# Kernel tuning notes

Measured on AMD Instinct MI355X. Metric: run time of the kernel, lower is better.

The kernel has to match this reference:

```python
import jax, jax.numpy as jnp
import numpy as np

INPUT_DIM = 1024
NUM_HEADS = 16


def setup_inputs() -> dict:
    key = jax.random.key(0)
    k1, k2, k3, k4, k5, k6, k7, k8 = jax.random.split(key, 8)
    bs, seq, dm = 2, 2048, INPUT_DIM
    scale = 1.0 / np.sqrt(dm)
    return {
        "input": jax.random.normal(k1, (bs, seq, dm), dtype=jnp.float32),
        "mask": jax.random.randint(k2, (bs, seq), 0, 2, dtype=jnp.int32),
        "Wq": jax.random.normal(k3, (dm, dm), dtype=jnp.float32) * scale,
        "bq": jax.random.normal(k4, (dm,), dtype=jnp.float32) * 0.01,
        "Wk": jax.random.normal(k5, (dm, dm), dtype=jnp.float32) * scale,
        "bk": jax.random.normal(k6, (dm,), dtype=jnp.float32) * 0.01,
        "Wv": jax.random.normal(k7, (dm, dm), dtype=jnp.float32) * scale,
        "bv": jax.random.normal(k8, (dm,), dtype=jnp.float32) * 0.01,
    }


def reference(input, mask, Wq, bq, Wk, bk, Wv, bv):
    bs, seq, dm = input.shape
    h = NUM_HEADS
    d = dm // h
    # projections: x @ W^T + b (torch Linear convention)
    Q = (input @ Wq.T + bq).reshape(bs, seq, h, d).transpose(0, 2, 1, 3)
    K = (input @ Wk.T + bk).reshape(bs, seq, h, d).transpose(0, 2, 1, 3)
    V = (input @ Wv.T + bv).reshape(bs, seq, h, d).transpose(0, 2, 1, 3)
    # raw scores [bs, h, seq, seq]
    scores = jnp.einsum("bhqd,bhkd->bhqk", Q, K)
    m = mask.astype(jnp.float32).reshape(bs, 1, 1, seq)
    # mask_logits is applied BEFORE the 1/sqrt(d) scaling, as in source
    scores = scores * m + (1.0 - m) * (-1e30)
    scores = scores * (1.0 / np.sqrt(d))
    attn = jax.nn.softmax(scores, axis=-1)  # dropout = identity at eval
    out = jnp.einsum("bhqk,bhkd->bhqd", attn, V)
    return out.transpose(0, 2, 1, 3).reshape(bs, seq, dm)
```

## Files before the change

kernel.cpp:

```cpp
#include <hip/hip_runtime.h>
#include <stdint.h>
#include <stddef.h>

#define SEQ 2048
#define DM  1024
#define NH  16
#define BS  2
#define PPAD 72

typedef __attribute__((ext_vector_type(8)))  __bf16 bf16x8;
typedef __attribute__((ext_vector_type(4)))  __bf16 bf16x4;
typedef __attribute__((ext_vector_type(4)))  float  floatx4;
typedef __attribute__((ext_vector_type(16))) float  floatx16;
typedef __attribute__((ext_vector_type(4)))  unsigned int uintx4;
typedef __attribute__((ext_vector_type(4)))  unsigned short ushortx4;

#if __has_builtin(__builtin_amdgcn_exp2f)
#define EXP2(x) __builtin_amdgcn_exp2f(x)
#else
#define EXP2(x) __expf((x) * 0.6931471805599453f)
#endif

#define QSCALE 0.18033688011112042f
#define MBIAS_OK (-11.541560327111707f)

#define GLDS(g, s) __builtin_amdgcn_global_load_lds( \
    (const __attribute__((address_space(1))) void*)(g), \
    (__attribute__((address_space(3))) void*)(s), 16, 0, 0)

__device__ inline unsigned short f2bf(float f) {
  union { float f; unsigned int u; } a; a.f = f;
  unsigned int u = a.u;
  return (unsigned short)((u + 0x7fffu + ((u >> 16) & 1u)) >> 16);
}

__device__ inline bf16x8 ldb8(const unsigned short* p) { return *(const bf16x8*)p; }

__global__ __launch_bounds__(256) void prep(
    const float* __restrict__ x, const float* __restrict__ wq,
    const float* __restrict__ wk, const float* __restrict__ wv,
    const int* __restrict__ mask,
    unsigned short* __restrict__ Xb, unsigned short* __restrict__ Wb,
    float* __restrict__ mbias) {
  const int bid = blockIdx.x, t = threadIdx.x;
  if (bid < 7168) {
    const float* src; unsigned short* dst; int base;
    if (bid < 4096)      { src = x;  dst = Xb;            base = bid; }
    else if (bid < 5120) { src = wq; dst = Wb;            base = bid - 4096; }
    else if (bid < 6144) { src = wk; dst = Wb + 1048576;  base = bid - 5120; }
    else                 { src = wv; dst = Wb + 2097152;  base = bid - 6144; }
    const int i = base * 256 + t;
    floatx4 v = ((const floatx4*)src)[i];
    ushortx4 o;
    o.x = f2bf(v.x); o.y = f2bf(v.y); o.z = f2bf(v.z); o.w = f2bf(v.w);
    ((ushortx4*)dst)[i] = o;
  } else {
    const int i = (bid - 7168) * 256 + t;
    mbias[i] = mask[i] ? MBIAS_OK : -1.0e30f;
  }
}

__global__ __launch_bounds__(256, 3) void gemm_qkv(
    const unsigned short* __restrict__ Xb, const unsigned short* __restrict__ Wb,
    const float* __restrict__ bq, const float* __restrict__ bk, const float* __restrict__ bv,
    unsigned short* __restrict__ Qb, unsigned short* __restrict__ Kb,
    unsigned short* __restrict__ Vt)
{
  __shared__ alignas(16) unsigned short LB[16384];
  const int t = threadIdx.x;
  const int w = t >> 6, l = t & 63;
  const int lm = l & 15, lq = l >> 4;
  const int z = blockIdx.z;
  const size_t m0 = (size_t)blockIdx.y * 128;
  const size_t n0 = (size_t)blockIdx.x * 128;
  const unsigned short* W = Wb + (size_t)z * (1024 * 1024);
  const float* bias = (z == 0) ? bq : ((z == 1) ? bk : bv);
  const float sc = (z == 0) ? QSCALE : 1.0f;

  const int c0 = t, c1 = 256 + t;
  const int row0 = c0 >> 2, row1 = c1 >> 2;
  const int kq0 = (c0 & 3) ^ ((row0 >> 1) & 3);
  const int kq1 = (c1 & 3) ^ ((row1 >> 1) & 3);
  const unsigned short* gA0 = Xb + (m0 + row0) * 1024 + kq0 * 8;
  const unsigned short* gA1 = Xb + (m0 + row1) * 1024 + kq1 * 8;
  const unsigned short* gB0 = W + (n0 + row0) * 1024 + kq0 * 8;
  const unsigned short* gB1 = W + (n0 + row1) * 1024 + kq1 * 8;
  const int la0 = (0 * 256 + w * 64) * 8;
  const int la1 = (1 * 256 + w * 64) * 8;

  const int wr = (w >> 1) * 64, wc = (w & 1) * 64;
  const int sw = (lq ^ ((lm >> 1) & 3)) * 8;
  floatx4 acc[4][4] = {};

  GLDS(gA0, LB + la0);
  GLDS(gA1, LB + la1);
  GLDS(gB0, LB + 8192 + la0);
  GLDS(gB1, LB + 8192 + la1);
  __syncthreads();

  for (int it = 0; it < 32; ++it) {
    const int cur = it & 1;
    if (it < 31) {
      const int kn = (it + 1) * 32;
      const int nb = (cur ^ 1) * 4096;
      GLDS(gA0 + kn, LB + nb + la0);
      GLDS(gA1 + kn, LB + nb + la1);
      GLDS(gB0 + kn, LB + 8192 + nb + la0);
      GLDS(gB1 + kn, LB + 8192 + nb + la1);
    }
    const unsigned short* Ab = LB + cur * 4096;
    const unsigned short* Bb = LB + 8192 + cur * 4096;
    bf16x8 af[4], bfr[4];
#pragma unroll
    for (int i = 0; i < 4; i++) af[i] = ldb8(Ab + (wr + i * 16 + lm) * 32 + sw);
#pragma unroll
    for (int j = 0; j < 4; j++) bfr[j] = ldb8(Bb + (wc + j * 16 + lm) * 32 + sw);
#pragma unroll
    for (int i = 0; i < 4; i++)
#pragma unroll
      for (int j = 0; j < 4; j++)
        acc[i][j] = __builtin_amdgcn_mfma_f32_16x16x32_bf16(af[i], bfr[j], acc[i][j], 0, 0, 0);
    __syncthreads();
  }

  if (z < 2) {
    unsigned short* dst = (z == 0) ? Qb : Kb;
#pragma unroll
    for (int j = 0; j < 4; j++) {
      const int ncol = (int)n0 + wc + j * 16 + lm;
      const float bval = bias[ncol];
#pragma unroll
      for (int i = 0; i < 4; i++)
#pragma unroll
        for (int r = 0; r < 4; r++) {
          const int mrow = (int)m0 + wr + i * 16 + lq * 4 + r;
          dst[(size_t)mrow * 1024 + ncol] = f2bf((acc[i][j][r] + bval) * sc);
        }
    }
  } else {
#pragma unroll
    for (int j = 0; j < 4; j++) {
      const int nl = wc + j * 16 + lm;
      const float bval = bias[(int)n0 + nl];
#pragma unroll
      for (int i = 0; i < 4; i++)
#pragma unroll
        for (int r = 0; r < 4; r++) {
          const int ml = wr + i * 16 + lq * 4 + r;
          LB[nl * 128 + ((((ml >> 3) ^ (nl & 15)) * 8) | (ml & 7))] = f2bf(acc[i][j][r] + bval);
        }
    }
    __syncthreads();
    const int nl = t >> 1, hf = t & 1;
    const int ncol = (int)n0 + nl;
    const int hh = ncol >> 6, dc = ncol & 63;
    const int bb = (int)(m0 >> 11);
    const int s0c = ((int)m0 & 2047) + hf * 64;
    unsigned short* dstp = Vt + (size_t)((bb * 16 + hh) * 64 + dc) * SEQ + s0c;
#pragma unroll
    for (int u = 0; u < 8; ++u) {
      const int phys = (hf * 8 + u) ^ (nl & 15);
      *(uintx4*)(dstp + u * 8) = *(const uintx4*)(LB + nl * 128 + phys * 8);
    }
  }
}

__global__ __launch_bounds__(256, 2) void attn(
    const unsigned short* __restrict__ Qb, const unsigned short* __restrict__ Kb,
    const unsigned short* __restrict__ Vt, const float* __restrict__ mbias,
    float* __restrict__ out)
{
  __shared__ alignas(16) unsigned short Klds[2][4096];
  __shared__ alignas(16) unsigned short Vlds[2][4096];
  __shared__ alignas(16) unsigned short Plds[4][32 * PPAD];
  __shared__ alignas(16) float Mlds[SEQ];

  const int t = threadIdx.x, w = t >> 6, l = t & 63;
  const int ln = l & 31, h = l >> 5;
  const int bid = blockIdx.x;
  const int pp = bid & 31;
  const int b = pp >> 4, head = pp & 15;
  const int q0w = (bid >> 5) * 128 + w * 32;
  const int hoff = head * 64;

  const int sr = l >> 3;
  const int gc = (l & 7) ^ sr;
  const unsigned short* gK[2]; const unsigned short* gV[2];
#pragma unroll
  for (int s2 = 0; s2 < 2; ++s2) {
    const int row = w * 16 + s2 * 8 + sr;
    gK[s2] = Kb + (size_t)(b * SEQ + row) * DM + hoff + gc * 8;
    gV[s2] = Vt + (size_t)((b * NH + head) * 64 + row) * SEQ + gc * 8;
  }

#pragma unroll
  for (int s2 = 0; s2 < 2; ++s2) {
    GLDS(gK[s2], &Klds[0][(w * 128 + s2 * 64) * 8]);
    GLDS(gV[s2], &Vlds[0][(w * 128 + s2 * 64) * 8]);
  }

  {
    const floatx4* mb4 = (const floatx4*)(mbias + b * SEQ);
    ((floatx4*)Mlds)[t] = mb4[t];
    ((floatx4*)Mlds)[256 + t] = mb4[256 + t];
  }

  const unsigned short* Qbase = Qb + (size_t)(b * SEQ + q0w + ln) * DM + hoff + h * 8;
  bf16x8 qf[4];
#pragma unroll
  for (int c = 0; c < 4; ++c) qf[c] = ldb8(Qbase + c * 16);

  const int cc = (ln >> 1) & 3, hb = h ^ (ln & 1);
  int xoff[4];
#pragma unroll
  for (int c = 0; c < 4; ++c) xoff[c] = (c ^ cc) * 16 + hb * 8;

  unsigned short* P = &Plds[w][ln * PPAD];
  floatx16 oacc[2] = {};
  float tsum = 0.0f;

  __syncthreads();

  for (int kt = 0; kt < 32; ++kt) {
    const int cur = kt & 1;
    if (kt < 31) {
      const int k0n = (kt + 1) * 64;
#pragma unroll
      for (int s2 = 0; s2 < 2; ++s2) {
        GLDS(gK[s2] + (size_t)k0n * DM, &Klds[cur ^ 1][(w * 128 + s2 * 64) * 8]);
        GLDS(gV[s2] + k0n,              &Vlds[cur ^ 1][(w * 128 + s2 * 64) * 8]);
      }
    }
    const unsigned short* Kc = &Klds[cur][ln * 64];
    const unsigned short* Vc = &Vlds[cur][ln * 64];

    bf16x8 kfr[8], vfr[8];
#pragma unroll
    for (int i = 0; i < 8; ++i) {
      kfr[i] = ldb8(Kc + (i >> 2) * 2048 + xoff[i & 3]);
      vfr[i] = ldb8(Vc + (i >> 2) * 2048 + xoff[i & 3]);
    }

    floatx16 s[2] = {};
#pragma unroll
    for (int c = 0; c < 4; ++c) {
      s[0] = __builtin_amdgcn_mfma_f32_32x32x16_bf16(kfr[c],     qf[c], s[0], 0, 0, 0);
      s[1] = __builtin_amdgcn_mfma_f32_32x32x16_bf16(kfr[4 + c], qf[c], s[1], 0, 0, 0);
    }

    const int k0 = kt * 64;
#pragma unroll
    for (int kb = 0; kb < 2; ++kb)
#pragma unroll
      for (int g = 0; g < 4; ++g) {
        const floatx4 mbv = *(const floatx4*)(Mlds + k0 + kb * 32 + g * 8 + h * 4);
        bf16x4 pk;
#pragma unroll
        for (int r = 0; r < 4; ++r) {
          const float pv = EXP2(s[kb][g * 4 + r] + mbv[r]);
          tsum += pv;
          pk[r] = (__bf16)pv;
        }
        *(bf16x4*)(P + kb * 32 + g * 8 + h * 4) = pk;
      }

    bf16x8 pf[4];
#pragma unroll
    for (int c = 0; c < 4; ++c) pf[c] = ldb8(P + c * 16 + h * 8);

#pragma unroll
    for (int c = 0; c < 4; ++c) {
      oacc[0] = __builtin_amdgcn_mfma_f32_32x32x16_bf16(pf[c], vfr[c],     oacc[0], 0, 0, 0);
      oacc[1] = __builtin_amdgcn_mfma_f32_32x32x16_bf16(pf[c], vfr[4 + c], oacc[1], 0, 0, 0);
    }
    __syncthreads();
  }

  tsum += __shfl_xor(tsum, 32, 64);
  const float inv = 1.0f / tsum;

  float* obase = out + (size_t)(b * SEQ + q0w) * DM + hoff;
#pragma unroll
  for (int r = 0; r < 16; ++r) {
    const int rq = (r & 3) + 8 * (r >> 2) + 4 * h;
    const float iv = __shfl(inv, rq, 64);
    obase[(size_t)rq * DM + ln]      = oacc[0][r] * iv;
    obase[(size_t)rq * DM + 32 + ln] = oacc[1][r] * iv;
  }
}

extern "C" void kernel_launch(void* const* d_in, const int* in_sizes, int n_in,
                              void* d_out, int out_size, void* d_ws, size_t ws_size,
                              hipStream_t stream) {
  const float* x   = (const float*)d_in[0];
  const int*   msk = (const int*)d_in[1];
  const float* Wq  = (const float*)d_in[2];
  const float* bq  = (const float*)d_in[3];
  const float* Wk  = (const float*)d_in[4];
  const float* bk  = (const float*)d_in[5];
  const float* Wv  = (const float*)d_in[6];
  const float* bv  = (const float*)d_in[7];
  float* out = (float*)d_out;

  unsigned short* ws = (unsigned short*)d_ws;
  unsigned short* Xb = ws;
  unsigned short* Wb = Xb + (size_t)4096 * 1024;
  unsigned short* Qb = Wb + (size_t)3 * 1024 * 1024;
  unsigned short* Kb = Qb + (size_t)4096 * 1024;
  unsigned short* Vt = Kb + (size_t)4096 * 1024;
  float* mbias = (float*)(Vt + (size_t)4096 * 1024);

  prep<<<7184, 256, 0, stream>>>(x, Wq, Wk, Wv, msk, Xb, Wb, mbias);

  gemm_qkv<<<dim3(8, 32, 3), 256, 0, stream>>>(Xb, Wb, bq, bk, bv, Qb, Kb, Vt);

  attn<<<512, 256, 0, stream>>>(Qb, Kb, Vt, mbias, out);
}
```

Measured before the change: 168.9 us.

## Fold key mask into V and compute softmax denominators with MFMA

The key mask is now applied in the V projection epilogue by zeroing V rows of masked keys. The attention loop therefore drops the per-element mask-bias add and the scalar running sum. Row sums of P are instead taken by an extra MFMA against a bf16 0/1 mask vector, so only unmasked keys enter the denominator. The P buffer is unpadded with an XOR swizzle and the mask buffer shrinks to bf16, which cuts LDS enough to raise occupancy to 3 blocks per CU. The cost is one extra MFMA per chunk, and exp2 now runs without the constant offset, which relies on the scores staying in range.

```diff
diff --git a/kernel.cpp b/kernel.cpp
--- a/kernel.cpp
+++ b/kernel.cpp
@@ -6,7 +6,6 @@
 #define DM  1024
 #define NH  16
 #define BS  2
-#define PPAD 72
 
 typedef __attribute__((ext_vector_type(8)))  __bf16 bf16x8;
 typedef __attribute__((ext_vector_type(4)))  __bf16 bf16x4;
@@ -22,7 +21,6 @@
 #endif
 
 #define QSCALE 0.18033688011112042f
-#define MBIAS_OK (-11.541560327111707f)
 
 #define GLDS(g, s) __builtin_amdgcn_global_load_lds( \
     (const __attribute__((address_space(1))) void*)(g), \
@@ -41,7 +39,7 @@
     const float* __restrict__ wk, const float* __restrict__ wv,
     const int* __restrict__ mask,
     unsigned short* __restrict__ Xb, unsigned short* __restrict__ Wb,
-    float* __restrict__ mbias) {
+    unsigned short* __restrict__ mb01) {
   const int bid = blockIdx.x, t = threadIdx.x;
   if (bid < 7168) {
     const float* src; unsigned short* dst; int base;
@@ -56,13 +54,14 @@
     ((ushortx4*)dst)[i] = o;
   } else {
     const int i = (bid - 7168) * 256 + t;
-    mbias[i] = mask[i] ? MBIAS_OK : -1.0e30f;
+    mb01[i] = mask[i] ? 0x3F80 : 0;
   }
 }
 
 __global__ __launch_bounds__(256, 3) void gemm_qkv(
     const unsigned short* __restrict__ Xb, const unsigned short* __restrict__ Wb,
     const float* __restrict__ bq, const float* __restrict__ bk, const float* __restrict__ bv,
+    const int* __restrict__ mask,
     unsigned short* __restrict__ Qb, unsigned short* __restrict__ Kb,
     unsigned short* __restrict__ Vt)
 {
@@ -138,6 +137,12 @@
         }
     }
   } else {
+    float mk[4][4];
+#pragma unroll
+    for (int i = 0; i < 4; i++)
+#pragma unroll
+      for (int r = 0; r < 4; r++)
+        mk[i][r] = (float)mask[(int)m0 + wr + i * 16 + lq * 4 + r];
 #pragma unroll
     for (int j = 0; j < 4; j++) {
       const int nl = wc + j * 16 + lm;
@@ -147,7 +152,8 @@
 #pragma unroll
         for (int r = 0; r < 4; r++) {
           const int ml = wr + i * 16 + lq * 4 + r;
-          LB[nl * 128 + ((((ml >> 3) ^ (nl & 15)) * 8) | (ml & 7))] = f2bf(acc[i][j][r] + bval);
+          LB[nl * 128 + ((((ml >> 3) ^ (nl & 15)) * 8) | (ml & 7))] =
+              f2bf((acc[i][j][r] + bval) * mk[i][r]);
         }
     }
     __syncthreads();
@@ -165,15 +171,15 @@
   }
 }
 
-__global__ __launch_bounds__(256, 2) void attn(
+__global__ __launch_bounds__(256, 3) void attn(
     const unsigned short* __restrict__ Qb, const unsigned short* __restrict__ Kb,
-    const unsigned short* __restrict__ Vt, const float* __restrict__ mbias,
+    const unsigned short* __restrict__ Vt, const unsigned short* __restrict__ mb01,
     float* __restrict__ out)
 {
   __shared__ alignas(16) unsigned short Klds[2][4096];
   __shared__ alignas(16) unsigned short Vlds[2][4096];
-  __shared__ alignas(16) unsigned short Plds[4][32 * PPAD];
-  __shared__ alignas(16) float Mlds[SEQ];
+  __shared__ alignas(16) unsigned short Plds[4][2048];
+  __shared__ alignas(16) unsigned short Mb[2048];
 
   const int t = threadIdx.x, w = t >> 6, l = t & 63;
   const int ln = l & 31, h = l >> 5;
@@ -199,11 +205,7 @@
     GLDS(gV[s2], &Vlds[0][(w * 128 + s2 * 64) * 8]);
   }
 
-  {
-    const floatx4* mb4 = (const floatx4*)(mbias + b * SEQ);
-    ((floatx4*)Mlds)[t] = mb4[t];
-    ((floatx4*)Mlds)[256 + t] = mb4[256 + t];
-  }
+  ((uintx4*)Mb)[t] = ((const uintx4*)(mb01 + b * SEQ))[t];
 
   const unsigned short* Qbase = Qb + (size_t)(b * SEQ + q0w + ln) * DM + hoff + h * 8;
   bf16x8 qf[4];
@@ -215,9 +217,9 @@
 #pragma unroll
   for (int c = 0; c < 4; ++c) xoff[c] = (c ^ cc) * 16 + hb * 8;
 
-  unsigned short* P = &Plds[w][ln * PPAD];
+  unsigned short* Pw = &Plds[w][ln * 64];
   floatx16 oacc[2] = {};
-  float tsum = 0.0f;
+  floatx16 tacc = {};
 
   __syncthreads();
 
@@ -248,25 +250,26 @@
       s[1] = __builtin_amdgcn_mfma_f32_32x32x16_bf16(kfr[4 + c], qf[c], s[1], 0, 0, 0);
     }
 
+#pragma unroll
+    for (int kb = 0; kb < 2; ++kb)
+#pragma unroll
+      for (int g = 0; g < 4; ++g) {
+        bf16x4 pk;
+#pragma unroll
+        for (int r = 0; r < 4; ++r) pk[r] = (__bf16)EXP2(s[kb][g * 4 + r]);
+        *(bf16x4*)(Pw + ((4 * kb + g) ^ (ln & 7)) * 8 + h * 4) = pk;
+      }
+
+    bf16x8 pf[4];
+#pragma unroll
+    for (int c = 0; c < 4; ++c) pf[c] = ldb8(Pw + xoff[c]);
+
     const int k0 = kt * 64;
 #pragma unroll
-    for (int kb = 0; kb < 2; ++kb)
-#pragma unroll
-      for (int g = 0; g < 4; ++g) {
-        const floatx4 mbv = *(const floatx4*)(Mlds + k0 + kb * 32 + g * 8 + h * 4);
-        bf16x4 pk;
-#pragma unroll
-        for (int r = 0; r < 4; ++r) {
-          const float pv = EXP2(s[kb][g * 4 + r] + mbv[r]);
-          tsum += pv;
-          pk[r] = (__bf16)pv;
-        }
-        *(bf16x4*)(P + kb * 32 + g * 8 + h * 4) = pk;
-      }
-
-    bf16x8 pf[4];
-#pragma unroll
-    for (int c = 0; c < 4; ++c) pf[c] = ldb8(P + c * 16 + h * 8);
+    for (int c = 0; c < 4; ++c) {
+      const bf16x8 mfr = ldb8(Mb + k0 + c * 16 + h * 8);
+      tacc = __builtin_amdgcn_mfma_f32_32x32x16_bf16(pf[c], mfr, tacc, 0, 0, 0);
+    }
 
 #pragma unroll
     for (int c = 0; c < 4; ++c) {
@@ -276,14 +279,11 @@
     __syncthreads();
   }
 
-  tsum += __shfl_xor(tsum, 32, 64);
-  const float inv = 1.0f / tsum;
-
   float* obase = out + (size_t)(b * SEQ + q0w) * DM + hoff;
 #pragma unroll
   for (int r = 0; r < 16; ++r) {
     const int rq = (r & 3) + 8 * (r >> 2) + 4 * h;
-    const float iv = __shfl(inv, rq, 64);
+    const float iv = __builtin_amdgcn_rcpf(tacc[r]);
     obase[(size_t)rq * DM + ln]      = oacc[0][r] * iv;
     obase[(size_t)rq * DM + 32 + ln] = oacc[1][r] * iv;
   }
@@ -308,11 +308,11 @@
   unsigned short* Qb = Wb + (size_t)3 * 1024 * 1024;
   unsigned short* Kb = Qb + (size_t)4096 * 1024;
   unsigned short* Vt = Kb + (size_t)4096 * 1024;
-  float* mbias = (float*)(Vt + (size_t)4096 * 1024);
-
-  prep<<<7184, 256, 0, stream>>>(x, Wq, Wk, Wv, msk, Xb, Wb, mbias);
-
-  gemm_qkv<<<dim3(8, 32, 3), 256, 0, stream>>>(Xb, Wb, bq, bk, bv, Qb, Kb, Vt);
-
-  attn<<<512, 256, 0, stream>>>(Qb, Kb, Vt, mbias, out);
-}
+  unsigned short* mb01 = Vt + (size_t)4096 * 1024;
+
+  prep<<<7184, 256, 0, stream>>>(x, Wq, Wk, Wv, msk, Xb, Wb, mb01);
+
+  gemm_qkv<<<dim3(8, 32, 3), 256, 0, stream>>>(Xb, Wb, bq, bk, bv, msk, Qb, Kb, Vt);
+
+  attn<<<512, 256, 0, stream>>>(Qb, Kb, Vt, mb01, out);
+}
```

Measured after the change: 170.5 us. About the same (+0.9%).
